# Kernel tuning notes

Measured on AMD Instinct MI355X. Metric: run time of the kernel, lower is better.

Reference implementation:

```python
import jax, jax.numpy as jnp
import numpy as np

MARGIN = 0.2


def _pdist_sq(x, y):
    # squared euclidean distances between rows of x [N,D] and rows of y [N,D] -> [N,N]
    xn = jnp.sum(x * x, axis=-1)
    yn = jnp.sum(y * y, axis=-1)
    d = xn[:, None] + yn[None, :] - 2.0 * (x @ y.T)
    return jnp.maximum(d, 0.0)


def _triplet_loss(embed1, embed2, margin):
    n = embed1.shape[0]
    # positive squared distance: dsq(e1_i, e2_i) == dsq(e2_i, e1_i)
    pos_sq = jnp.sum((embed1 - embed2) ** 2, axis=-1)      # [N]
    d_pos = jnp.sqrt(pos_sq)                                # [N], anchor-positive L2

    D11 = _pdist_sq(embed1, embed1)                         # [N,N]
    D12 = _pdist_sq(embed1, embed2)
    D21 = D12.T
    D22 = _pdist_sq(embed2, embed2)

    offdiag = ~jnp.eye(n, dtype=bool)
    p = pos_sq[:, None]
    # four mining cases from the original nested loop (anchor, pos, neg):
    #  A: (e1_i, e2_i, e1_j) if dsq(e1_i,e2_i) < dsq(e1_i,e1_j)
    #  B: (e1_i, e2_i, e2_j) if dsq(e1_i,e2_i) < dsq(e1_i,e2_j)
    #  C: (e2_i, e1_i, e1_j) if dsq(e2_i,e1_i) < dsq(e2_i,e1_j)
    #  D: (e2_i, e1_i, e2_j) if dsq(e2_i,e1_i) < dsq(e2_i,e2_j)
    masks = [ (p < D11) & offdiag,
              (p < D12) & offdiag,
              (p < D21) & offdiag,
              (p < D22) & offdiag ]
    negs = [D11, D12, D21, D22]

    total = jnp.float32(0.0)
    count = jnp.float32(0.0)
    for m, Dn in zip(masks, negs):
        d_neg = jnp.sqrt(jnp.where(m, Dn, 1.0))  # where() keeps sqrt grad finite on masked zeros
        hinge = jnp.maximum(margin + d_pos[:, None] - d_neg, 0.0)
        total = total + jnp.sum(jnp.where(m, hinge, 0.0))
        count = count + jnp.sum(m).astype(jnp.float32)
    # TripletMarginLoss reduction='mean' over the mined triplets
    return total / jnp.maximum(count, 1.0)


def setup_inputs() -> dict:
    key = jax.random.key(0)
    k1, k2 = jax.random.split(key)
    N, D = 4096, 512
    embed1 = jax.random.normal(k1, (N, D), dtype=jnp.float32)
    embed2 = jax.random.normal(k2, (N, D), dtype=jnp.float32)
    return {"embed1": embed1, "embed2": embed2}


def reference(embed1, embed2):
    return _triplet_loss(embed1, embed2, MARGIN)
```

## Files before the change

kernel.cpp:

```cpp
#include <hip/hip_runtime.h>
#include <cstdint>

#define MARGIN_F 0.2f

typedef __attribute__((ext_vector_type(4))) float fv4;
typedef __attribute__((ext_vector_type(2))) long lv2;

__device__ __forceinline__ void gload16(const void* g, void* l) {
    __builtin_amdgcn_global_load_lds(
        (const __attribute__((address_space(1))) unsigned*)g,
        (__attribute__((address_space(3))) unsigned*)l,
        16, 0, 0);
}

__global__ __launch_bounds__(128) void prep_kernel(
    const float* __restrict__ e1, const float* __restrict__ e2,
    unsigned* __restrict__ e1q, unsigned* __restrict__ e2q,
    float* __restrict__ n1, float* __restrict__ n2, float* __restrict__ dpos)
{
    const int row = blockIdx.x;
    const int t = threadIdx.x;
    const float4 a = reinterpret_cast<const float4*>(e1 + (size_t)row * 512)[t];
    const float4 b = reinterpret_cast<const float4*>(e2 + (size_t)row * 512)[t];

    int pa = __builtin_amdgcn_cvt_pk_fp8_f32(a.x, a.y, 0, false);
    pa     = __builtin_amdgcn_cvt_pk_fp8_f32(a.z, a.w, pa, true);
    int pb = __builtin_amdgcn_cvt_pk_fp8_f32(b.x, b.y, 0, false);
    pb     = __builtin_amdgcn_cvt_pk_fp8_f32(b.z, b.w, pb, true);

    const int wq    = t >> 5;
    const int u     = t & 31;
    const int blk   = u >> 1;
    const int piece = u & 1;
    const int tb    = ((blk >> 3) << 3) | ((blk & 3) << 1) | ((blk >> 2) & 1);
    const int di    = (wq << 5) + (tb << 1) + piece;
    e1q[row * 128 + di] = (unsigned)pa;
    e2q[row * 128 + di] = (unsigned)pb;

    float s1 = a.x*a.x + a.y*a.y + a.z*a.z + a.w*a.w;
    float s2 = b.x*b.x + b.y*b.y + b.z*b.z + b.w*b.w;
    float dx = a.x-b.x, dy = a.y-b.y, dz = a.z-b.z, dw = a.w-b.w;
    float sp = dx*dx + dy*dy + dz*dz + dw*dw;

    #pragma unroll
    for (int o = 32; o; o >>= 1) {
        s1 += __shfl_down(s1, o);
        s2 += __shfl_down(s2, o);
        sp += __shfl_down(sp, o);
    }
    __shared__ float r1[2], r2[2], rp[2];
    if ((t & 63) == 0) { int wv = t >> 6; r1[wv] = s1; r2[wv] = s2; rp[wv] = sp; }
    __syncthreads();
    if (t == 0) {
        n1[row] = r1[0] + r1[1];
        n2[row] = r2[0] + r2[1];
        dpos[row] = sqrtf(rp[0] + rp[1]);
    }
}

__global__ __launch_bounds__(256, 3) void triplet_main(
    const unsigned char* __restrict__ e1q, const unsigned char* __restrict__ e2q,
    const float* __restrict__ n1, const float* __restrict__ n2,
    const float* __restrict__ dpos,
    float* __restrict__ total, unsigned* __restrict__ count)
{
    __shared__ char buf[32768];
    __shared__ float scRN[128], scRD[128], scCN[128], scCD[128];
    __shared__ float lt[4];
    __shared__ unsigned lc[4];

    const int bid = blockIdx.x;
    int bi, bjStart, ntiles, flavor;
    if (bid < 256) {
        flavor = 0; bi = bid >> 3; bjStart = (bid & 7) << 2; ntiles = 4;
    } else {
        int b = bid - 256; flavor = 1;
        if (b >= 144) { b -= 144; flavor = 2; }
        int r = 0;
        while (b >= ((35 - r) >> 2)) { b -= (35 - r) >> 2; ++r; }
        bi = r; bjStart = r + (b << 2);
        ntiles = 32 - bjStart; if (ntiles > 4) ntiles = 4;
    }
    const int i0 = bi << 7;
    const char* Xc = (const char*)((flavor == 2) ? e2q : e1q);
    const char* Yc = (const char*)((flavor == 1) ? e1q : e2q);
    const float* nR = (flavor == 2) ? n2 : n1;
    const float* nC = (flavor == 1) ? n1 : n2;

    const int tid  = threadIdx.x;
    const int w    = tid >> 6;
    const int lane = tid & 63;
    const int l15  = lane & 15;
    const int l4   = lane >> 4;
    const int wr   = w >> 1;
    const int wc   = w & 1;

    long srcA[4];
    #pragma unroll
    for (int c = 0; c < 4; ++c) {
        const int chA = tid + (c << 8);
        const int rA  = chA >> 3;
        srcA[c] = (long)(i0 + rA) * 512 + (((chA & 7) << 4) ^ ((rA & 7) << 4));
    }
    const int ldst = w << 10;

#define STAGE(T, JD) do {                                                    \
    const long kb_ = (long)(T) << 7;                                         \
    _Pragma("unroll")                                                        \
    for (int c = 0; c < 4; ++c) {                                            \
        gload16(Xc + srcA[c] + kb_,        buf + (c << 12) + ldst);          \
        gload16(Yc + srcA[c] + (JD) + kb_, buf + 16384 + (c << 12) + ldst);  \
    }                                                                        \
} while (0)

    const int slot = (l4 << 4) ^ ((l15 & 7) << 4);
    const int aB = ((wr << 6) + l15) * 128 + slot;
    const int bB = 16384 + ((wc << 6) + l15) * 128 + slot;

#define EPI(EMITCOL, NEEDNEQ) do {                                           \
    float cN_[4], cM_[4];                                                    \
    _Pragma("unroll")                                                        \
    for (int n = 0; n < 4; ++n) {                                            \
        const int cl = (wc << 6) + (n << 4) + l15;                           \
        cN_[n] = scCN[cl]; cM_[n] = scCD[cl] + MARGIN_F;                     \
    }                                                                        \
    _Pragma("unroll")                                                        \
    for (int m = 0; m < 4; ++m) {                                            \
        _Pragma("unroll")                                                    \
        for (int rr = 0; rr < 4; ++rr) {                                     \
            const int rl = (wr << 6) + (m << 4) + (l4 << 2) + rr;            \
            const float rN = scRN[rl];                                       \
            const float rM = scRD[rl] + MARGIN_F;                            \
            _Pragma("unroll")                                                \
            for (int n = 0; n < 4; ++n) {                                    \
                const float D = fmaxf(fmaf(-2.0f, acc[m][n][rr],             \
                                           rN + cN_[n]), 0.0f);              \
                const float s = __builtin_amdgcn_sqrtf(D);                   \
                bool neq = true;                                             \
                if (NEEDNEQ) neq = (rl != ((wc << 6) + (n << 4) + l15));     \
                const float t1 = rM - s;                                     \
                const bool c1 = (t1 < MARGIN_F) && neq;                      \
                lcnt += c1;                                                  \
                ltot += c1 ? fmaxf(t1, 0.0f) : 0.0f;                         \
                if (EMITCOL) {                                               \
                    const float t2 = cM_[n] - s;                             \
                    const bool c2 = (t2 < MARGIN_F) && neq;                  \
                    lcnt += c2;                                              \
                    ltot += c2 ? fmaxf(t2, 0.0f) : 0.0f;                     \
                }                                                            \
            }                                                                \
        }                                                                    \
    }                                                                        \
} while (0)

    const int j0first = bjStart << 7;
    if (tid < 128)      { scRN[tid] = nR[i0 + tid]; scRD[tid] = dpos[i0 + tid]; }
    else { const int t = tid - 128; scCN[t] = nC[j0first + t]; scCD[t] = dpos[j0first + t]; }
    STAGE(0, (long)(j0first - i0) * 512);

    float    ltot = 0.0f;
    unsigned lcnt = 0;
    fv4 acc[4][4];

    for (int tt = 0; tt < ntiles; ++tt) {
        const int j0   = (bjStart + tt) << 7;
        const long jd  = (long)(j0 - i0) * 512;
        const bool last = (tt + 1 >= ntiles);
        const bool needNeq = (i0 == j0);

        #pragma unroll
        for (int m = 0; m < 4; ++m)
            #pragma unroll
            for (int n = 0; n < 4; ++n) acc[m][n] = (fv4)0.0f;

        for (int t = 0; t < 4; ++t) {
            __syncthreads();
            #pragma unroll
            for (int h = 0; h < 2; ++h) {
                const int H = h << 6;
                lv2 a_[4], b_[4];
                #pragma unroll
                for (int m = 0; m < 4; ++m)
                    a_[m] = *(const lv2*)(buf + ((aB + m * 2048) ^ H));
                #pragma unroll
                for (int n = 0; n < 4; ++n)
                    b_[n] = *(const lv2*)(buf + ((bB + n * 2048) ^ H));
                #pragma unroll
                for (int m = 0; m < 4; ++m)
                    #pragma unroll
                    for (int n = 0; n < 4; ++n) {
                        acc[m][n] = __builtin_amdgcn_mfma_f32_16x16x32_fp8_fp8(
                            a_[m][0], b_[n][0], acc[m][n], 0, 0, 0);
                        acc[m][n] = __builtin_amdgcn_mfma_f32_16x16x32_fp8_fp8(
                            a_[m][1], b_[n][1], acc[m][n], 0, 0, 0);
                    }
            }
            __syncthreads();
            if (t < 3)      STAGE(t + 1, jd);
            else if (!last) STAGE(0, jd + 65536);
        }

        if (!needNeq)           EPI(true, false);
        else if (flavor == 0)   EPI(true, true);
        else                    EPI(false, true);

        if (!last) {
            __syncthreads();
            if (tid >= 128) {
                const int t2 = tid - 128;
                scCN[t2] = nC[j0 + 128 + t2]; scCD[t2] = dpos[j0 + 128 + t2];
            }
        }
    }
#undef STAGE
#undef EPI

    #pragma unroll
    for (int o = 32; o; o >>= 1) {
        ltot += __shfl_down(ltot, o);
        lcnt += __shfl_down(lcnt, o);
    }
    __syncthreads();
    if (lane == 0) { lt[w] = ltot; lc[w] = lcnt; }
    __syncthreads();
    if (tid == 0) {
        float T = 0.0f; unsigned C = 0;
        #pragma unroll
        for (int x = 0; x < 4; ++x) { T += lt[x]; C += lc[x]; }
        atomicAdd(total, T);
        atomicAdd(count, C);
    }
}

__global__ void finalize_kernel(const float* __restrict__ total,
                                const unsigned* __restrict__ count,
                                float* __restrict__ out)
{
    out[0] = total[0] / fmaxf((float)count[0], 1.0f);
}

extern "C" void kernel_launch(void* const* d_in, const int* in_sizes, int n_in,
                              void* d_out, int out_size, void* d_ws, size_t ws_size,
                              hipStream_t stream) {
    const float* e1 = (const float*)d_in[0];
    const float* e2 = (const float*)d_in[1];
    char* ws = (char*)d_ws;

    float*    total = (float*)ws;
    unsigned* count = (unsigned*)(ws + 4);
    float* n1   = (float*)(ws + 1024);
    float* n2   = n1 + 4096;
    float* dpos = n2 + 4096;
    unsigned* e1q = (unsigned*)(ws + (1 << 17));
    unsigned* e2q = e1q + (size_t)4096 * 128;

    hipMemsetAsync(ws, 0, 64, stream);
    prep_kernel<<<4096, 128, 0, stream>>>(e1, e2, e1q, e2q, n1, n2, dpos);
    triplet_main<<<544, 256, 0, stream>>>((const unsigned char*)e1q,
                                          (const unsigned char*)e2q,
                                          n1, n2, dpos, total, count);
    finalize_kernel<<<1, 1, 0, stream>>>(total, count, (float*)d_out);
}
```

Baseline: 67.98 us.

## Process column tiles in pairs to reuse A fragments across 128x256 block tiles

The main loop now stages two adjacent 128-column B tiles at once and runs a 4x8 MFMA accumulator grid. Each A fragment loaded from LDS is reused across twice as many columns, and there are half as many barriers per column tile. Odd tile counts use a single-tile first group. The cost is 48KB of LDS and doubled accumulator registers, with occupancy lowered from 3 to 2 blocks per CU, which may reduce latency hiding.

```diff
diff --git a/kernel.cpp b/kernel.cpp
--- a/kernel.cpp
+++ b/kernel.cpp
@@ -58,14 +58,14 @@
     }
 }
 
-__global__ __launch_bounds__(256, 3) void triplet_main(
+__global__ __launch_bounds__(256, 2) void triplet_main(
     const unsigned char* __restrict__ e1q, const unsigned char* __restrict__ e2q,
     const float* __restrict__ n1, const float* __restrict__ n2,
     const float* __restrict__ dpos,
     float* __restrict__ total, unsigned* __restrict__ count)
 {
-    __shared__ char buf[32768];
-    __shared__ float scRN[128], scRD[128], scCN[128], scCD[128];
+    __shared__ char buf[49152];
+    __shared__ float scRN[128], scRD[128], scCN[256], scCD[256];
     __shared__ float lt[4];
     __shared__ unsigned lc[4];
 
@@ -104,7 +104,7 @@
     }
     const int ldst = w << 10;
 
-#define STAGE(T, JD) do {                                                    \
+#define STAGE_S(T, JD) do {                                                  \
     const long kb_ = (long)(T) << 7;                                         \
     _Pragma("unroll")                                                        \
     for (int c = 0; c < 4; ++c) {                                            \
@@ -113,16 +113,29 @@
     }                                                                        \
 } while (0)
 
+#define STAGE_P(T, JD) do {                                                  \
+    const long kb_ = (long)(T) << 7;                                         \
+    _Pragma("unroll")                                                        \
+    for (int c = 0; c < 4; ++c) {                                            \
+        gload16(Xc + srcA[c] + kb_,                buf + (c << 12) + ldst);          \
+        gload16(Yc + srcA[c] + (JD) + kb_,         buf + 16384 + (c << 12) + ldst);  \
+        gload16(Yc + srcA[c] + (JD) + 65536 + kb_, buf + 32768 + (c << 12) + ldst);  \
+    }                                                                        \
+} while (0)
+
     const int slot = (l4 << 4) ^ ((l15 & 7) << 4);
     const int aB = ((wr << 6) + l15) * 128 + slot;
     const int bB = 16384 + ((wc << 6) + l15) * 128 + slot;
 
-#define EPI(EMITCOL, NEEDNEQ) do {                                           \
+    fv4 acc[4][8];
+
+#define EPI(EMITCOL, NEEDNEQ, P) do {                                        \
     float cN_[4], cM_[4];                                                    \
     _Pragma("unroll")                                                        \
     for (int n = 0; n < 4; ++n) {                                            \
         const int cl = (wc << 6) + (n << 4) + l15;                           \
-        cN_[n] = scCN[cl]; cM_[n] = scCD[cl] + MARGIN_F;                     \
+        cN_[n] = scCN[cl + ((P) << 7)];                                      \
+        cM_[n] = scCD[cl + ((P) << 7)] + MARGIN_F;                           \
     }                                                                        \
     _Pragma("unroll")                                                        \
     for (int m = 0; m < 4; ++m) {                                            \
@@ -133,7 +146,7 @@
             const float rM = scRD[rl] + MARGIN_F;                            \
             _Pragma("unroll")                                                \
             for (int n = 0; n < 4; ++n) {                                    \
-                const float D = fmaxf(fmaf(-2.0f, acc[m][n][rr],             \
+                const float D = fmaxf(fmaf(-2.0f, acc[m][n + ((P) << 2)][rr],\
                                            rN + cN_[n]), 0.0f);              \
                 const float s = __builtin_amdgcn_sqrtf(D);                   \
                 bool neq = true;                                             \
@@ -153,67 +166,113 @@
     }                                                                        \
 } while (0)
 
-    const int j0first = bjStart << 7;
-    if (tid < 128)      { scRN[tid] = nR[i0 + tid]; scRD[tid] = dpos[i0 + tid]; }
-    else { const int t = tid - 128; scCN[t] = nC[j0first + t]; scCD[t] = dpos[j0first + t]; }
-    STAGE(0, (long)(j0first - i0) * 512);
+#define EPIDISPATCH(P, J0P) do {                                             \
+    const bool nn_ = (i0 == (J0P));                                          \
+    if (!nn_)             EPI(true, false, P);                               \
+    else if (flavor == 0) EPI(true, true, P);                                \
+    else                  EPI(false, true, P);                               \
+} while (0)
+
+    bool gPair = ((ntiles & 1) == 0);
+    int  tt = 0;
+    int  jbase = bjStart << 7;
+    {
+        int gj = jbase + tid; if (gj > 4095) gj = 4095;
+        scCN[tid] = nC[gj]; scCD[tid] = dpos[gj];
+        if (tid < 128) { scRN[tid] = nR[i0 + tid]; scRD[tid] = dpos[i0 + tid]; }
+    }
+    {
+        const long jd0 = (long)(jbase - i0) * 512;
+        if (gPair) STAGE_P(0, jd0); else STAGE_S(0, jd0);
+    }
 
     float    ltot = 0.0f;
     unsigned lcnt = 0;
-    fv4 acc[4][4];
-
-    for (int tt = 0; tt < ntiles; ++tt) {
-        const int j0   = (bjStart + tt) << 7;
-        const long jd  = (long)(j0 - i0) * 512;
-        const bool last = (tt + 1 >= ntiles);
-        const bool needNeq = (i0 == j0);
+
+    for (;;) {
+        const int  gsize   = gPair ? 2 : 1;
+        const int  ttn     = tt + gsize;
+        const bool hasNext = (ttn < ntiles);
+        const long jd      = (long)(jbase - i0) * 512;
+        const long jdn     = (long)(((bjStart + ttn) << 7) - i0) * 512;
 
         #pragma unroll
         for (int m = 0; m < 4; ++m)
             #pragma unroll
-            for (int n = 0; n < 4; ++n) acc[m][n] = (fv4)0.0f;
+            for (int n = 0; n < 8; ++n) acc[m][n] = (fv4)0.0f;
 
         for (int t = 0; t < 4; ++t) {
             __syncthreads();
-            #pragma unroll
-            for (int h = 0; h < 2; ++h) {
-                const int H = h << 6;
-                lv2 a_[4], b_[4];
+            if (gPair) {
                 #pragma unroll
-                for (int m = 0; m < 4; ++m)
-                    a_[m] = *(const lv2*)(buf + ((aB + m * 2048) ^ H));
+                for (int h = 0; h < 2; ++h) {
+                    const int H = h << 6;
+                    lv2 a_[4], b_[8];
+                    #pragma unroll
+                    for (int m = 0; m < 4; ++m)
+                        a_[m] = *(const lv2*)(buf + ((aB + m * 2048) ^ H));
+                    #pragma unroll
+                    for (int n = 0; n < 4; ++n) {
+                        b_[n]     = *(const lv2*)(buf + ((bB + n * 2048) ^ H));
+                        b_[4 + n] = *(const lv2*)(buf + ((bB + 16384 + n * 2048) ^ H));
+                    }
+                    #pragma unroll
+                    for (int m = 0; m < 4; ++m)
+                        #pragma unroll
+                        for (int n = 0; n < 8; ++n) {
+                            acc[m][n] = __builtin_amdgcn_mfma_f32_16x16x32_fp8_fp8(
+                                a_[m][0], b_[n][0], acc[m][n], 0, 0, 0);
+                            acc[m][n] = __builtin_amdgcn_mfma_f32_16x16x32_fp8_fp8(
+                                a_[m][1], b_[n][1], acc[m][n], 0, 0, 0);
+                        }
+                }
+            } else {
                 #pragma unroll
-                for (int n = 0; n < 4; ++n)
-                    b_[n] = *(const lv2*)(buf + ((bB + n * 2048) ^ H));
-                #pragma unroll
-                for (int m = 0; m < 4; ++m)
-                    #pragma unroll
-                    for (int n = 0; n < 4; ++n) {
-                        acc[m][n] = __builtin_amdgcn_mfma_f32_16x16x32_fp8_fp8(
-                            a_[m][0], b_[n][0], acc[m][n], 0, 0, 0);
-                        acc[m][n] = __builtin_amdgcn_mfma_f32_16x16x32_fp8_fp8(
-                            a_[m][1], b_[n][1], acc[m][n], 0, 0, 0);
-                    }
+                for (int h = 0; h < 2; ++h) {
+                    const int H = h << 6;
+                    lv2 a_[4], b_[4];
+                    #pragma unroll
+                    for (int m = 0; m < 4; ++m)
+                        a_[m] = *(const lv2*)(buf + ((aB + m * 2048) ^ H));
+                    #pragma unroll
+                    for (int n = 0; n < 4; ++n)
+                        b_[n] = *(const lv2*)(buf + ((bB + n * 2048) ^ H));
+                    #pragma unroll
+                    for (int m = 0; m < 4; ++m)
+                        #pragma unroll
+                        for (int n = 0; n < 4; ++n) {
+                            acc[m][n] = __builtin_amdgcn_mfma_f32_16x16x32_fp8_fp8(
+                                a_[m][0], b_[n][0], acc[m][n], 0, 0, 0);
+                            acc[m][n] = __builtin_amdgcn_mfma_f32_16x16x32_fp8_fp8(
+                                a_[m][1], b_[n][1], acc[m][n], 0, 0, 0);
+                        }
+                }
             }
             __syncthreads();
-            if (t < 3)      STAGE(t + 1, jd);
-            else if (!last) STAGE(0, jd + 65536);
-        }
-
-        if (!needNeq)           EPI(true, false);
-        else if (flavor == 0)   EPI(true, true);
-        else                    EPI(false, true);
-
-        if (!last) {
-            __syncthreads();
-            if (tid >= 128) {
-                const int t2 = tid - 128;
-                scCN[t2] = nC[j0 + 128 + t2]; scCD[t2] = dpos[j0 + 128 + t2];
+            if (t < 3) {
+                if (gPair) STAGE_P(t + 1, jd); else STAGE_S(t + 1, jd);
+            } else if (hasNext) {
+                STAGE_P(0, jdn);
             }
         }
-    }
-#undef STAGE
+
+        EPIDISPATCH(0, jbase);
+        if (gPair) EPIDISPATCH(1, jbase + 128);
+
+        if (!hasNext) break;
+
+        __syncthreads();
+        jbase = (bjStart + ttn) << 7;
+        {
+            int gj = jbase + tid; if (gj > 4095) gj = 4095;
+            scCN[tid] = nC[gj]; scCD[tid] = dpos[gj];
+        }
+        tt = ttn; gPair = true;
+    }
+#undef STAGE_S
+#undef STAGE_P
 #undef EPI
+#undef EPIDISPATCH
 
     #pragma unroll
     for (int o = 32; o; o >>= 1) {
```

Result: slower. 81.17 us (+19.4%).
